# Performance work log

Measured on AMD Instinct MI355X. Metric: run time of the kernel, lower is better.

## Reference

```python
import jax, jax.numpy as jnp
import numpy as np

MARGIN = 0.0  # init kwarg margin=0


def setup_inputs() -> dict:
    key = jax.random.key(0)
    k1, k2 = jax.random.split(key)
    inputs = jax.random.normal(k1, (4096, 2048), dtype=jnp.float32)
    targets = jax.random.randint(k2, (4096,), 0, 64, dtype=jnp.int64)
    return {"inputs": inputs, "targets": targets}


def _last_true_index(cond):
    # cond: (n, n) bool. Original torch loop zeros leading True entries until one
    # remains -> keeps the LAST True index per row.
    n = cond.shape[1]
    return (n - 1) - jnp.argmax(cond[:, ::-1], axis=1)


def reference(inputs, targets):
    n = inputs.shape[0]
    INF = jnp.asarray(jnp.inf, dtype=inputs.dtype)

    # pairwise euclidean distances: ||xi||^2 + ||xj||^2 - 2 xi.xj, clamp, sqrt
    sq = jnp.sum(inputs * inputs, axis=1)
    dist = sq[:, None] + sq[None, :] - 2.0 * (inputs @ inputs.T)
    dist = jnp.sqrt(jnp.clip(dist, 1e-12))  # (n, n)

    same = targets[:, None] == targets[None, :]  # (n, n) same-label mask

    # hardest positive / hardest negative per row
    dist_ap = jnp.where(same, dist, -INF).max(axis=1)
    dist_an = jnp.where(same, INF, dist).min(axis=1)

    # tie-broken indices (last occurrence, matching the torch loop)
    p = _last_true_index((dist == dist_ap[:, None]) & same)      # hardest pos idx
    q = _last_true_index((dist == dist_an[:, None]) & (~same))   # hardest neg idx

    # an2 = dist(hardest_pos_i, hardest_neg_i)
    dist_an2 = dist[p, q]

    # maskc: labels differing from both anchor's label and hardest-negative's label
    lbl_q = targets[q]
    maskc = (targets[None, :] != targets[:, None]) & (targets[None, :] != lbl_q[:, None])

    dist_q = dist[q]  # (n, n): distance rows of the hardest negatives
    ok_min = jnp.where(maskc, dist_q, INF).min(axis=1)
    r = _last_true_index((dist_q == ok_min[:, None]) & maskc)

    dist_an3 = dist[jnp.arange(n), r]  # dist(anchor, third-class sample)
    dist_an4 = dist_q[jnp.arange(n), r]  # dist(hardest neg, third-class sample) == ok_min

    # MarginRankingLoss(margin, reduce=False) with y=1: relu(ap - an + margin)
    loss = jax.nn.relu(dist_ap - dist_an + MARGIN)
    loss3 = jnp.abs(dist_an - dist_an2)
    loss4 = jnp.abs(dist_an3 - dist_an4)
    return (loss + loss3 + loss4).sum() / n
```

## Files before the change

### kernel.cpp

```cpp
#include <hip/hip_runtime.h>
#include <hip/hip_bf16.h>
#include <cstdint>

#define N_DIM 4096
#define K_DIM 2048
#define NKT 32
#define QSCALE 24.0f
#define QINV (1.0f / 24.0f)

typedef float floatx4 __attribute__((ext_vector_type(4)));
typedef int intx4 __attribute__((ext_vector_type(4)));
typedef unsigned short ushort8 __attribute__((ext_vector_type(8)));
typedef unsigned long long ull;

__device__ __forceinline__ unsigned short f2bf(float f) {
    unsigned int u = __builtin_bit_cast(unsigned int, f);
    unsigned int r = (u + 0x7fffu + ((u >> 16) & 1u)) >> 16;
    return (unsigned short)r;
}

__device__ __forceinline__ float bf2f(unsigned short b) {
    return __uint_as_float(((unsigned)b) << 16);
}

__device__ __forceinline__ void gld_lds16(const void* g, void* l) {
    __builtin_amdgcn_global_load_lds(
        (const __attribute__((address_space(1))) unsigned int*)g,
        (__attribute__((address_space(3))) unsigned int*)l,
        16, 0, 0);
}

__global__ __launch_bounds__(256)
void prep_kernel(const float* __restrict__ X, char* __restrict__ Qt,
                 int* __restrict__ sqi) {
    const int row = blockIdx.x;
    const int tid = threadIdx.x;
    const float* xr = X + (size_t)row * K_DIM;
    floatx4 a = *(const floatx4*)(xr + tid * 8);
    floatx4 b = *(const floatx4*)(xr + tid * 8 + 4);
    int s = 0;
    unsigned lo = 0, hi = 0;
#pragma unroll
    for (int e = 0; e < 4; ++e) {
        int v = __float2int_rn(a[e] * QSCALE);
        v = min(127, max(-127, v));
        s += v * v;
        lo |= ((unsigned)(v & 0xff)) << (8 * e);
        int w = __float2int_rn(b[e] * QSCALE);
        w = min(127, max(-127, w));
        s += w * w;
        hi |= ((unsigned)(w & 0xff)) << (8 * e);
    }
    *(int2*)(Qt + ((size_t)(tid >> 1) * 4096 + row) * 16 + (tid & 1) * 8) =
        make_int2((int)lo, (int)hi);
#pragma unroll
    for (int off = 32; off; off >>= 1) s += __shfl_down(s, off);
    __shared__ int wsum[4];
    const int wave = tid >> 6, lane = tid & 63;
    if (lane == 0) wsum[wave] = s;
    __syncthreads();
    if (tid == 0) sqi[row] = wsum[0] + wsum[1] + wsum[2] + wsum[3];
}

#define BAR() { __builtin_amdgcn_s_barrier(); asm volatile("" ::: "memory"); }
#define PRIO1() __builtin_amdgcn_s_setprio(1)
#define PRIO0() __builtin_amdgcn_s_setprio(0)
#define VMCNT5() { asm volatile("s_waitcnt vmcnt(5)" ::: "memory"); \
                   __builtin_amdgcn_sched_barrier(0); }
#define VMCNT0() { asm volatile("s_waitcnt vmcnt(0)" ::: "memory"); \
                   __builtin_amdgcn_sched_barrier(0); }
#define KTB 262144
#define LOAD_A(DST) { \
    asm volatile("global_load_dwordx4 %0, %1, off"            : "=&v"(DST[0]) : "v"(aAddr)); \
    asm volatile("global_load_dwordx4 %0, %1, off offset:256" : "=&v"(DST[1]) : "v"(aAddr)); \
    asm volatile("global_load_dwordx4 %0, %1, off offset:512" : "=&v"(DST[2]) : "v"(aAddr)); \
    asm volatile("global_load_dwordx4 %0, %1, off offset:768" : "=&v"(DST[3]) : "v"(aAddr)); \
    aAddr += KTB; }
#define MM16(AF) { _Pragma("unroll") for (int n_ = 0; n_ < 4; ++n_) { \
    _Pragma("unroll") for (int m_ = 0; m_ < 4; ++m_) { \
        acc[n_][m_] = __builtin_amdgcn_mfma_i32_16x16x64_i8( \
            AF[m_], bfv[n_], acc[n_][m_], 0, 0, 0); } } }
#define TILE_BODY(T, LD, USE) { \
    if ((T) < NKT - 1) LOAD_A(LD); \
    if ((T) < NKT - 1) { VMCNT5(); } else { VMCNT0(); } \
    BAR(); \
    if ((T) < NKT - 2) gld_lds16(bSrc + (size_t)((T) + 2) * KTB, lds + sb + widB); \
    _Pragma("unroll") \
    for (int n_ = 0; n_ < 4; ++n_) bfv[n_] = *(const intx4*)(lds + cb + rB[n_]); \
    PRIO1(); MM16(USE); PRIO0(); \
    cb += 8192; if (cb >= 24576) cb = 0; \
    sb += 8192; if (sb >= 24576) sb = 0; }

__global__ __launch_bounds__(512, 4)
void gemm_dist(const char* __restrict__ Qt, const int* __restrict__ sqi,
               unsigned short* __restrict__ Db) {
    __shared__ char lds[24576];
    const int tid = threadIdx.x;
    const int wid = tid >> 6, lane = tid & 63;
    const int wr = wid >> 1, wc = wid & 1;
    const int fr = lane & 15, ksub = lane >> 4;
    const int widB = wid * 1024;

    int rB[4];
#pragma unroll
    for (int n = 0; n < 4; ++n) rB[n] = (ksub * 128 + wc * 64 + n * 16 + fr) * 16;

    const int xcd = blockIdx.x & 7, kk = blockIdx.x >> 3;
    const int bi = (kk >> 3) | ((xcd & 1) << 3);
    const int bj = (kk & 7) | ((xcd >> 1) << 3);
    const int rowC0 = bi * 256, colC0 = bj * 128;

    unsigned long long aAddr = (unsigned long long)(Qt +
        ((size_t)ksub * 4096 + rowC0 + wr * 64 + fr) * 16);
    const char* bSrc = Qt + ((size_t)(tid >> 7) * 4096 + colC0 + (tid & 127)) * 16;

    intx4 acc[4][4];
#pragma unroll
    for (int a1 = 0; a1 < 4; ++a1)
#pragma unroll
    for (int a2 = 0; a2 < 4; ++a2) acc[a1][a2] = (intx4){0, 0, 0, 0};
    intx4 afX[4], afY[4], bfv[4];

    LOAD_A(afX);
    gld_lds16(bSrc,       lds + 0    + widB);
    gld_lds16(bSrc + KTB, lds + 8192 + widB);

    int cb = 0, sb = 16384;
#pragma unroll 1
    for (int it = 0; it < NKT / 2; ++it) {
        const int t0 = it * 2;
        TILE_BODY(t0,     afY, afX);
        TILE_BODY(t0 + 1, afX, afY);
    }

#pragma unroll
    for (int n = 0; n < 4; ++n) {
        const int col = colC0 + wc * 64 + n * 16 + fr;
        const int sqc = sqi[col];
#pragma unroll
        for (int m = 0; m < 4; ++m) {
            const int row0 = rowC0 + wr * 64 + m * 16 + ksub * 4;
#pragma unroll
            for (int r = 0; r < 4; ++r) {
                const int v = sqi[row0 + r] + sqc - 2 * acc[n][m][r];
                const float d = (v > 0) ? sqrtf((float)v) * QINV : 1e-6f;
                Db[(size_t)(row0 + r) * N_DIM + col] = f2bf(d);
            }
        }
    }
}

__global__ __launch_bounds__(256)
void stats_loss(const unsigned short* __restrict__ Db, const int* __restrict__ tgt,
                float* __restrict__ lossArr) {
    const int i = blockIdx.x, tid = threadIdx.x;
    const int ti = tgt[i];
    const unsigned short* row = Db + (size_t)i * N_DIM;
    ull kmax = 0ULL, kmin = ~0ULL;
#pragma unroll
    for (int it = 0; it < 2; ++it) {
        const int j0 = (it * 256 + tid) * 8;
        ushort8 d = *(const ushort8*)(row + j0);
        intx4 ta = *(const intx4*)(tgt + j0);
        intx4 tb = *(const intx4*)(tgt + j0 + 4);
#pragma unroll
        for (int e = 0; e < 8; ++e) {
            const int j = j0 + e;
            const int tl = (e < 4) ? ta[e] : tb[e - 4];
            const ull db = (ull)d[e] << 32;
            if (tl == ti) { ull k = db | (unsigned)j;  if (k > kmax) kmax = k; }
            else          { ull k = db | (unsigned)~j; if (k < kmin) kmin = k; }
        }
    }
    __shared__ ull sM[256], sN[256];
    sM[tid] = kmax; sN[tid] = kmin;
    __syncthreads();
    for (int off = 128; off; off >>= 1) {
        if (tid < off) {
            if (sM[tid + off] > sM[tid]) sM[tid] = sM[tid + off];
            if (sN[tid + off] < sN[tid]) sN[tid] = sN[tid + off];
        }
        __syncthreads();
    }
    const ull km = sM[0], kn = sN[0];
    const float ap = bf2f((unsigned short)(km >> 32));
    const int p = (int)(unsigned)(km & 0xFFFFFFFFu);
    const float an = bf2f((unsigned short)(kn >> 32));
    const int q = (int)~(unsigned)(kn & 0xFFFFFFFFu);
    __syncthreads();

    const int lq = tgt[q];
    const unsigned short* rowq = Db + (size_t)q * N_DIM;
    ull kr = ~0ULL;
#pragma unroll
    for (int it = 0; it < 2; ++it) {
        const int j0 = (it * 256 + tid) * 8;
        ushort8 d = *(const ushort8*)(rowq + j0);
        intx4 ta = *(const intx4*)(tgt + j0);
        intx4 tb = *(const intx4*)(tgt + j0 + 4);
#pragma unroll
        for (int e = 0; e < 8; ++e) {
            const int j = j0 + e;
            const int tl = (e < 4) ? ta[e] : tb[e - 4];
            if (tl != ti && tl != lq) {
                ull k = ((ull)d[e] << 32) | (unsigned)~j;
                if (k < kr) kr = k;
            }
        }
    }
    sN[tid] = kr;
    __syncthreads();
    for (int off = 128; off; off >>= 1) {
        if (tid < off) { if (sN[tid + off] < sN[tid]) sN[tid] = sN[tid + off]; }
        __syncthreads();
    }
    if (tid == 0) {
        const ull kk = sN[0];
        const float okmin = bf2f((unsigned short)(kk >> 32));
        const int r = (int)~(unsigned)(kk & 0xFFFFFFFFu);
        const float an2 = bf2f(Db[(size_t)p * N_DIM + q]);
        const float an3 = bf2f(Db[(size_t)i * N_DIM + r]);
        lossArr[i] = fmaxf(ap - an, 0.f) + fabsf(an - an2) + fabsf(an3 - okmin);
    }
}

__global__ __launch_bounds__(256)
void finred(const float* __restrict__ lossArr, float* __restrict__ out) {
    const int tid = threadIdx.x;
    float s = 0.f;
    for (int j = tid; j < N_DIM; j += 256) s += lossArr[j];
#pragma unroll
    for (int off = 32; off; off >>= 1) s += __shfl_down(s, off);
    __shared__ float w[4];
    const int wave = tid >> 6, lane = tid & 63;
    if (lane == 0) w[wave] = s;
    __syncthreads();
    if (tid == 0) out[0] = (w[0] + w[1] + w[2] + w[3]) * (1.0f / (float)N_DIM);
}

extern "C" void kernel_launch(void* const* d_in, const int* in_sizes, int n_in,
                              void* d_out, int out_size, void* d_ws, size_t ws_size,
                              hipStream_t stream) {
    const float* X = (const float*)d_in[0];
    const int* tgt = (const int*)d_in[1];
    float* out = (float*)d_out;

    char* w = (char*)d_ws;
    char* Qt = w;
    unsigned short* Db = (unsigned short*)(w + ((size_t)16 << 20));
    int* sqi = (int*)(w + ((size_t)80 << 20));
    float* lossArr = (float*)(sqi + N_DIM);

    prep_kernel<<<N_DIM, 256, 0, stream>>>(X, Qt, sqi);
    gemm_dist<<<512, 512, 0, stream>>>(Qt, sqi, Db);
    stats_loss<<<N_DIM, 256, 0, stream>>>(Db, tgt, lossArr);
    finred<<<1, 256, 0, stream>>>(lossArr, out);
}
```

Measured before the change: 78.90 us.

## Fuse per-row hardest pos/neg reduction into GEMM epilogue with 4-wave blocks

The GEMM kernel moves from 8 waves of 64x64 tiles to 4 waves that each own 64x128 (8x4 MFMA accumulators), staging B with two LDS copies per thread. Its epilogue also computes per-row partial max-same-label and min-other-label keys over each 128-column tile and writes them to Gmax/Gmin buffers. stats_loss then reduces 32 partials per row instead of rescanning the full distance row. This removes one full read of the 32MB bf16 distance matrix. The cost is higher register pressure, lower occupancy and a larger LDS footprint in the GEMM.

```diff
diff --git a/kernel.cpp b/kernel.cpp
--- a/kernel.cpp
+++ b/kernel.cpp
@@ -65,7 +65,7 @@
 #define BAR() { __builtin_amdgcn_s_barrier(); asm volatile("" ::: "memory"); }
 #define PRIO1() __builtin_amdgcn_s_setprio(1)
 #define PRIO0() __builtin_amdgcn_s_setprio(0)
-#define VMCNT5() { asm volatile("s_waitcnt vmcnt(5)" ::: "memory"); \
+#define VMCNT6() { asm volatile("s_waitcnt vmcnt(6)" ::: "memory"); \
                    __builtin_amdgcn_sched_barrier(0); }
 #define VMCNT0() { asm volatile("s_waitcnt vmcnt(0)" ::: "memory"); \
                    __builtin_amdgcn_sched_barrier(0); }
@@ -76,34 +76,37 @@
     asm volatile("global_load_dwordx4 %0, %1, off offset:512" : "=&v"(DST[2]) : "v"(aAddr)); \
     asm volatile("global_load_dwordx4 %0, %1, off offset:768" : "=&v"(DST[3]) : "v"(aAddr)); \
     aAddr += KTB; }
-#define MM16(AF) { _Pragma("unroll") for (int n_ = 0; n_ < 4; ++n_) { \
+#define STG_B(KT, BB) { \
+    gld_lds16(bSrc + (size_t)(KT) * KTB,          lds + (BB) + widB); \
+    gld_lds16(bSrc + (size_t)(KT) * KTB + 131072, lds + (BB) + 4096 + widB); }
+#define MM32(AF) { _Pragma("unroll") for (int n_ = 0; n_ < 8; ++n_) { \
     _Pragma("unroll") for (int m_ = 0; m_ < 4; ++m_) { \
         acc[n_][m_] = __builtin_amdgcn_mfma_i32_16x16x64_i8( \
             AF[m_], bfv[n_], acc[n_][m_], 0, 0, 0); } } }
 #define TILE_BODY(T, LD, USE) { \
     if ((T) < NKT - 1) LOAD_A(LD); \
-    if ((T) < NKT - 1) { VMCNT5(); } else { VMCNT0(); } \
+    if ((T) < NKT - 1) { VMCNT6(); } else { VMCNT0(); } \
     BAR(); \
-    if ((T) < NKT - 2) gld_lds16(bSrc + (size_t)((T) + 2) * KTB, lds + sb + widB); \
+    if ((T) < NKT - 2) STG_B((T) + 2, sb); \
     _Pragma("unroll") \
-    for (int n_ = 0; n_ < 4; ++n_) bfv[n_] = *(const intx4*)(lds + cb + rB[n_]); \
-    PRIO1(); MM16(USE); PRIO0(); \
+    for (int n_ = 0; n_ < 8; ++n_) bfv[n_] = *(const intx4*)(lds + cb + rB[n_]); \
+    PRIO1(); MM32(USE); PRIO0(); \
     cb += 8192; if (cb >= 24576) cb = 0; \
     sb += 8192; if (sb >= 24576) sb = 0; }
 
-__global__ __launch_bounds__(512, 4)
+__global__ __launch_bounds__(256, 2)
 void gemm_dist(const char* __restrict__ Qt, const int* __restrict__ sqi,
-               unsigned short* __restrict__ Db) {
-    __shared__ char lds[24576];
+               const int* __restrict__ tgt, unsigned short* __restrict__ Db,
+               ull* __restrict__ Gmax, ull* __restrict__ Gmin) {
+    __shared__ char lds[65536];
     const int tid = threadIdx.x;
     const int wid = tid >> 6, lane = tid & 63;
-    const int wr = wid >> 1, wc = wid & 1;
     const int fr = lane & 15, ksub = lane >> 4;
     const int widB = wid * 1024;
 
-    int rB[4];
-#pragma unroll
-    for (int n = 0; n < 4; ++n) rB[n] = (ksub * 128 + wc * 64 + n * 16 + fr) * 16;
+    int rB[8];
+#pragma unroll
+    for (int n = 0; n < 8; ++n) rB[n] = (ksub * 128 + n * 16 + fr) * 16;
 
     const int xcd = blockIdx.x & 7, kk = blockIdx.x >> 3;
     const int bi = (kk >> 3) | ((xcd & 1) << 3);
@@ -111,19 +114,19 @@
     const int rowC0 = bi * 256, colC0 = bj * 128;
 
     unsigned long long aAddr = (unsigned long long)(Qt +
-        ((size_t)ksub * 4096 + rowC0 + wr * 64 + fr) * 16);
+        ((size_t)ksub * 4096 + rowC0 + wid * 64 + fr) * 16);
     const char* bSrc = Qt + ((size_t)(tid >> 7) * 4096 + colC0 + (tid & 127)) * 16;
 
-    intx4 acc[4][4];
-#pragma unroll
-    for (int a1 = 0; a1 < 4; ++a1)
+    intx4 acc[8][4];
+#pragma unroll
+    for (int a1 = 0; a1 < 8; ++a1)
 #pragma unroll
     for (int a2 = 0; a2 < 4; ++a2) acc[a1][a2] = (intx4){0, 0, 0, 0};
-    intx4 afX[4], afY[4], bfv[4];
+    intx4 afX[4], afY[4], bfv[8];
 
     LOAD_A(afX);
-    gld_lds16(bSrc,       lds + 0    + widB);
-    gld_lds16(bSrc + KTB, lds + 8192 + widB);
+    STG_B(0, 0);
+    STG_B(1, 8192);
 
     int cb = 0, sb = 16384;
 #pragma unroll 1
@@ -133,61 +136,73 @@
         TILE_BODY(t0 + 1, afX, afY);
     }
 
-#pragma unroll
-    for (int n = 0; n < 4; ++n) {
-        const int col = colC0 + wc * 64 + n * 16 + fr;
-        const int sqc = sqi[col];
-#pragma unroll
-        for (int m = 0; m < 4; ++m) {
-            const int row0 = rowC0 + wr * 64 + m * 16 + ksub * 4;
-#pragma unroll
-            for (int r = 0; r < 4; ++r) {
-                const int v = sqi[row0 + r] + sqc - 2 * acc[n][m][r];
+    BAR();
+    ull* sMax = (ull*)lds;
+    ull* sMin = (ull*)(lds + 32768);
+    int tc[8];
+#pragma unroll
+    for (int n = 0; n < 8; ++n) tc[n] = tgt[colC0 + n * 16 + fr];
+#pragma unroll
+    for (int m = 0; m < 4; ++m) {
+#pragma unroll
+        for (int r = 0; r < 4; ++r) {
+            const int rowL = wid * 64 + m * 16 + ksub * 4 + r;
+            const int row = rowC0 + rowL;
+            const int sqr = sqi[row];
+            const int tr = tgt[row];
+            ull kmx = 0ULL, kmn = ~0ULL;
+#pragma unroll
+            for (int n = 0; n < 8; ++n) {
+                const int col = colC0 + n * 16 + fr;
+                const int v = sqr + sqi[col] - 2 * acc[n][m][r];
                 const float d = (v > 0) ? sqrtf((float)v) * QINV : 1e-6f;
-                Db[(size_t)(row0 + r) * N_DIM + col] = f2bf(d);
+                const unsigned short db16 = f2bf(d);
+                Db[(size_t)row * N_DIM + col] = db16;
+                const ull db = (ull)db16 << 32;
+                if (tc[n] == tr) { ull k = db | (unsigned)col;  if (k > kmx) kmx = k; }
+                else             { ull k = db | (unsigned)~col; if (k < kmn) kmn = k; }
             }
-        }
+            sMax[rowL * 16 + fr] = kmx;
+            sMin[rowL * 16 + fr] = kmn;
+        }
+    }
+    BAR();
+    {
+        const ull* rm = sMax + tid * 16;
+        const ull* rn = sMin + tid * 16;
+        ull km = rm[0], kn = rn[0];
+#pragma unroll
+        for (int e = 1; e < 16; ++e) {
+            if (rm[e] > km) km = rm[e];
+            if (rn[e] < kn) kn = rn[e];
+        }
+        Gmax[(size_t)(rowC0 + tid) * 32 + bj] = km;
+        Gmin[(size_t)(rowC0 + tid) * 32 + bj] = kn;
     }
 }
 
 __global__ __launch_bounds__(256)
 void stats_loss(const unsigned short* __restrict__ Db, const int* __restrict__ tgt,
+                const ull* __restrict__ Gmax, const ull* __restrict__ Gmin,
                 float* __restrict__ lossArr) {
     const int i = blockIdx.x, tid = threadIdx.x;
     const int ti = tgt[i];
-    const unsigned short* row = Db + (size_t)i * N_DIM;
-    ull kmax = 0ULL, kmin = ~0ULL;
-#pragma unroll
-    for (int it = 0; it < 2; ++it) {
-        const int j0 = (it * 256 + tid) * 8;
-        ushort8 d = *(const ushort8*)(row + j0);
-        intx4 ta = *(const intx4*)(tgt + j0);
-        intx4 tb = *(const intx4*)(tgt + j0 + 4);
-#pragma unroll
-        for (int e = 0; e < 8; ++e) {
-            const int j = j0 + e;
-            const int tl = (e < 4) ? ta[e] : tb[e - 4];
-            const ull db = (ull)d[e] << 32;
-            if (tl == ti) { ull k = db | (unsigned)j;  if (k > kmax) kmax = k; }
-            else          { ull k = db | (unsigned)~j; if (k < kmin) kmin = k; }
-        }
-    }
-    __shared__ ull sM[256], sN[256];
-    sM[tid] = kmax; sN[tid] = kmin;
-    __syncthreads();
-    for (int off = 128; off; off >>= 1) {
-        if (tid < off) {
-            if (sM[tid + off] > sM[tid]) sM[tid] = sM[tid + off];
-            if (sN[tid + off] < sN[tid]) sN[tid] = sN[tid + off];
+    __shared__ ull sM[32], sN2[32];
+    if (tid < 32) sM[tid] = Gmax[(size_t)i * 32 + tid];
+    else if (tid < 64) sN2[tid - 32] = Gmin[(size_t)i * 32 + (tid - 32)];
+    __syncthreads();
+    for (int off = 16; off; off >>= 1) {
+        if (tid < off) { if (sM[tid + off] > sM[tid]) sM[tid] = sM[tid + off]; }
+        else if (tid >= 32 && tid < 32 + off) {
+            if (sN2[tid - 32 + off] < sN2[tid - 32]) sN2[tid - 32] = sN2[tid - 32 + off];
         }
         __syncthreads();
     }
-    const ull km = sM[0], kn = sN[0];
+    const ull km = sM[0], kn = sN2[0];
     const float ap = bf2f((unsigned short)(km >> 32));
     const int p = (int)(unsigned)(km & 0xFFFFFFFFu);
     const float an = bf2f((unsigned short)(kn >> 32));
     const int q = (int)~(unsigned)(kn & 0xFFFFFFFFu);
-    __syncthreads();
 
     const int lq = tgt[q];
     const unsigned short* rowq = Db + (size_t)q * N_DIM;
@@ -208,14 +223,15 @@
             }
         }
     }
-    sN[tid] = kr;
+    __shared__ ull sR[256];
+    sR[tid] = kr;
     __syncthreads();
     for (int off = 128; off; off >>= 1) {
-        if (tid < off) { if (sN[tid + off] < sN[tid]) sN[tid] = sN[tid + off]; }
+        if (tid < off) { if (sR[tid + off] < sR[tid]) sR[tid] = sR[tid + off]; }
         __syncthreads();
     }
     if (tid == 0) {
-        const ull kk = sN[0];
+        const ull kk = sR[0];
         const float okmin = bf2f((unsigned short)(kk >> 32));
         const int r = (int)~(unsigned)(kk & 0xFFFFFFFFu);
         const float an2 = bf2f(Db[(size_t)p * N_DIM + q]);
@@ -250,9 +266,11 @@
     unsigned short* Db = (unsigned short*)(w + ((size_t)16 << 20));
     int* sqi = (int*)(w + ((size_t)80 << 20));
     float* lossArr = (float*)(sqi + N_DIM);
+    ull* Gmax = (ull*)(w + ((size_t)82 << 20));
+    ull* Gmin = Gmax + (size_t)N_DIM * 32;
 
     prep_kernel<<<N_DIM, 256, 0, stream>>>(X, Qt, sqi);
-    gemm_dist<<<512, 512, 0, stream>>>(Qt, sqi, Db);
-    stats_loss<<<N_DIM, 256, 0, stream>>>(Db, tgt, lossArr);
+    gemm_dist<<<512, 256, 0, stream>>>(Qt, sqi, tgt, Db, Gmax, Gmin);
+    stats_loss<<<N_DIM, 256, 0, stream>>>(Db, tgt, Gmax, Gmin, lossArr);
     finred<<<1, 256, 0, stream>>>(lossArr, out);
 }
```

Measured after the change: 84.25 us. 1.07x slower.
